# Kernel optimization log

Hardware: AMD Instinct MI355X
Metric: run time of the kernel (lower is better)

Reference implementation:

```python
import jax, jax.numpy as jnp
import numpy as np

BETA = 0.1
EPS_LOW = 0.2
EPS_HIGH = 0.2
TEMPERATURE = 1.0
H, V = 1024, 32000
B, T = 4, 1024


def _per_token_logps(hidden, weight, ids):
    # hidden: [B,T,H], weight: [V,H], ids: [B,T] -> gathered log-softmax logps [B,T]
    logits = jnp.einsum('bth,vh->btv', hidden, weight) / TEMPERATURE  # [B,T,V]
    lse = jax.nn.logsumexp(logits, axis=-1)                            # [B,T]
    sel = jnp.take_along_axis(logits, ids[..., None], axis=-1)[..., 0]
    return sel - lse


def setup_inputs() -> dict:
    key = jax.random.key(0)
    k1, k2, k3, k4, k5, k6 = jax.random.split(key, 6)
    x = jax.random.normal(k1, (B, T, H), dtype=jnp.float32)
    ref_input = jax.random.normal(k2, (B, T, H), dtype=jnp.float32)
    # lm-head weights (policy and frozen reference), scaled like nn.Linear init
    weight = jax.random.normal(k3, (V, H), dtype=jnp.float32) * (1.0 / np.sqrt(H))
    ref_weight = jax.random.normal(k4, (V, H), dtype=jnp.float32) * (1.0 / np.sqrt(H))
    selected_token_ids = jax.random.randint(k5, (B, T), 0, V, dtype=jnp.int32)
    attention_mask = jnp.ones((B, T), dtype=jnp.int32)
    advantages = jax.random.normal(k6, (B,), dtype=jnp.float32)
    return {
        'x': x,
        'weight': weight,
        'ref_input': ref_input,
        'ref_weight': ref_weight,
        'advantages': advantages,
        'selected_token_ids': selected_token_ids,
        'attention_mask': attention_mask,
    }


def reference(x, weight, ref_input, ref_weight, advantages, selected_token_ids, attention_mask):
    # policy per-token logps
    logps = _per_token_logps(x, weight, selected_token_ids)  # [B,T]
    # reference model logps (no grad path in original)
    ref_logps = jax.lax.stop_gradient(
        _per_token_logps(ref_input, ref_weight, selected_token_ids))
    # old logps default: detached current logps -> ratio = 1 in forward
    old_logps = jax.lax.stop_gradient(logps)

    log_ratio = logps - old_logps
    coef_1 = jnp.exp(log_ratio)
    coef_2 = jnp.clip(coef_1, 1.0 - EPS_LOW, 1.0 + EPS_HIGH)
    adv = advantages[:, None]  # [B,1]
    per_token_loss = -jnp.minimum(coef_1 * adv, coef_2 * adv)

    # KL penalty to reference model: exp(ref-cur) - (ref-cur) - 1
    d = ref_logps - logps
    kl = jnp.exp(d) - d - 1.0
    per_token_loss = per_token_loss + BETA * kl

    mask = attention_mask.astype(per_token_loss.dtype)
    # loss_type 'bnpo': batch-normalized policy optimization
    loss = jnp.sum(per_token_loss * mask) / jnp.maximum(jnp.sum(mask), 1.0)
    return loss
```

## Files before the change

### kernel.cpp

```cpp
#include <hip/hip_runtime.h>
#include <hip/hip_bf16.h>
#include <math.h>

constexpr int kH   = 1024;
constexpr int kV   = 32000;
constexpr int kTok = 4096;
constexpr int BM   = 256;
constexpr int BN   = 256;
constexpr int BK   = 64;
constexpr int NT   = kH / BK;
constexpr int NVT  = kV / BN;
constexpr int NMT  = kTok / BM;

typedef _Float16 f16x8 __attribute__((ext_vector_type(8)));
typedef float    f32x4 __attribute__((ext_vector_type(4)));

typedef __attribute__((address_space(1))) const void gvoid_t;
typedef __attribute__((address_space(3))) void lvoid_t;

__global__ __launch_bounds__(256) void convert_kernel(
    const float* __restrict__ src, _Float16* __restrict__ dst)
{
  int idx = blockIdx.x * 256 + threadIdx.x;
  int row = idx >> 7;
  int blk = idx & 127;
  int chunk = blk >> 3;
  int c = blk & 7;
  int p = c ^ (row & 7);
  const float* s = src + ((size_t)row << 10) + (blk << 3);
  float4 v0 = *(const float4*)s;
  float4 v1 = *(const float4*)(s + 4);
  f16x8 o = { (_Float16)v0.x, (_Float16)v0.y, (_Float16)v0.z, (_Float16)v0.w,
              (_Float16)v1.x, (_Float16)v1.y, (_Float16)v1.z, (_Float16)v1.w };
  *(f16x8*)&dst[((size_t)row << 10) + (chunk << 6) + (p << 3)] = o;
}

__global__ __launch_bounds__(512, 2) void lse_gemm_kernel(
    const _Float16* __restrict__ X0, const _Float16* __restrict__ W0,
    const _Float16* __restrict__ X1, const _Float16* __restrict__ W1,
    float2* __restrict__ P0, float2* __restrict__ P1)
{
  __shared__ _Float16 lds[2][2][BM * BK];

  const _Float16* Xp = blockIdx.z ? X1 : X0;
  const _Float16* Wp = blockIdx.z ? W1 : W0;
  float2* Pp = blockIdx.z ? P1 : P0;

  const int tid  = threadIdx.x;
  const int wave = tid >> 6;
  const int lane = tid & 63;
  const int quad = lane >> 4;
  const int lc   = lane & 15;
  const int wr   = wave >> 2;
  const int wc   = wave & 3;
  const int srow = lane >> 3;
  const int sblk = lane & 7;

  const int m_base = blockIdx.x * BM;
  const int v_base = blockIdx.y * BN;

  const _Float16* gA = Xp + (size_t)(m_base + wave * 8 + srow) * kH + sblk * 8;
  const _Float16* gB = Wp + (size_t)(v_base + wave * 8 + srow) * kH + sblk * 8;

  const int xb0 = ((quad       ^ (lc & 7)) << 3);
  const int xb1 = (((quad + 4) ^ (lc & 7)) << 3);
  const int rA0 = (wr * 128 + lc) * BK;
  const int rB0 = (wc * 64  + lc) * BK;

  f32x4 acc[8][4];
#pragma unroll
  for (int i = 0; i < 8; ++i)
#pragma unroll
    for (int j = 0; j < 4; ++j) acc[i][j] = (f32x4){0.f, 0.f, 0.f, 0.f};

  f16x8 bf[4][2];

#define STG_A(c, kt, h) do {                                                        \
    __builtin_amdgcn_global_load_lds(                                               \
        (gvoid_t*)(gA + (size_t)((h) * 128     ) * kH + (kt) * BK),                 \
        (lvoid_t*)&lds[c][0][(((h) * 128     ) + wave * 8) * BK], 16, 0, 0);        \
    __builtin_amdgcn_global_load_lds(                                               \
        (gvoid_t*)(gA + (size_t)((h) * 128 + 64) * kH + (kt) * BK),                 \
        (lvoid_t*)&lds[c][0][(((h) * 128 + 64) + wave * 8) * BK], 16, 0, 0);        \
  } while (0)
#define STG_B(c, kt, h) do {                                                        \
    __builtin_amdgcn_global_load_lds(                                               \
        (gvoid_t*)(gB + (size_t)((h) * 128     ) * kH + (kt) * BK),                 \
        (lvoid_t*)&lds[c][1][(((h) * 128     ) + wave * 8) * BK], 16, 0, 0);        \
    __builtin_amdgcn_global_load_lds(                                               \
        (gvoid_t*)(gB + (size_t)((h) * 128 + 64) * kH + (kt) * BK),                 \
        (lvoid_t*)&lds[c][1][(((h) * 128 + 64) + wave * 8) * BK], 16, 0, 0);        \
  } while (0)

#define VM6  asm volatile("s_waitcnt vmcnt(6)" ::: "memory")
#define VM0  asm volatile("s_waitcnt vmcnt(0)" ::: "memory")
#define NOP_ ((void)0)

#define PH(c, g, S, V) do {                                                         \
    if ((g) == 0) {                                                                 \
      _Pragma("unroll")                                                             \
      for (int j = 0; j < 4; ++j) {                                                 \
        bf[j][0] = *(const f16x8*)&lds[c][1][rB0 + j * 1024 + xb0];                 \
        bf[j][1] = *(const f16x8*)&lds[c][1][rB0 + j * 1024 + xb1];                 \
      }                                                                             \
    }                                                                               \
    f16x8 a00 = *(const f16x8*)&lds[c][0][rA0 + (g) * 2048 +        xb0];           \
    f16x8 a01 = *(const f16x8*)&lds[c][0][rA0 + (g) * 2048 +        xb1];           \
    f16x8 a10 = *(const f16x8*)&lds[c][0][rA0 + (g) * 2048 + 1024 + xb0];           \
    f16x8 a11 = *(const f16x8*)&lds[c][0][rA0 + (g) * 2048 + 1024 + xb1];           \
    S;                                                                              \
    V;                                                                              \
    __builtin_amdgcn_s_barrier();                                                   \
    __builtin_amdgcn_s_setprio(1);                                                  \
    _Pragma("unroll")                                                               \
    for (int j = 0; j < 4; ++j) {                                                   \
      acc[(g)*2  ][j] = __builtin_amdgcn_mfma_f32_16x16x32_f16(bf[j][0], a00, acc[(g)*2  ][j], 0, 0, 0); \
      acc[(g)*2  ][j] = __builtin_amdgcn_mfma_f32_16x16x32_f16(bf[j][1], a01, acc[(g)*2  ][j], 0, 0, 0); \
      acc[(g)*2+1][j] = __builtin_amdgcn_mfma_f32_16x16x32_f16(bf[j][0], a10, acc[(g)*2+1][j], 0, 0, 0); \
      acc[(g)*2+1][j] = __builtin_amdgcn_mfma_f32_16x16x32_f16(bf[j][1], a11, acc[(g)*2+1][j], 0, 0, 0); \
    }                                                                               \
    __builtin_amdgcn_s_setprio(0);                                                  \
    __builtin_amdgcn_s_barrier();                                                   \
  } while (0)

  STG_B(0, 0, 0); STG_B(0, 0, 1); STG_A(0, 0, 0); STG_A(0, 0, 1);
  STG_B(1, 1, 0); STG_B(1, 1, 1); STG_A(1, 1, 0);
  VM6;
  __builtin_amdgcn_s_barrier();

  for (int kt = 0; kt < NT - 2; kt += 2) {
    PH(0, 0, STG_A(1, kt + 1, 1), NOP_);
    PH(0, 1, STG_B(0, kt + 2, 0), NOP_);
    PH(0, 2, STG_B(0, kt + 2, 1), NOP_);
    PH(0, 3, STG_A(0, kt + 2, 0), VM6);
    PH(1, 0, STG_A(0, kt + 2, 1), NOP_);
    PH(1, 1, STG_B(1, kt + 3, 0), NOP_);
    PH(1, 2, STG_B(1, kt + 3, 1), NOP_);
    PH(1, 3, STG_A(1, kt + 3, 0), VM6);
  }
  PH(0, 0, STG_A(1, NT - 1, 1), NOP_);
  PH(0, 1, NOP_, NOP_);
  PH(0, 2, NOP_, NOP_);
  PH(0, 3, NOP_, VM0);
  PH(1, 0, NOP_, NOP_);
  PH(1, 1, NOP_, NOP_);
  PH(1, 2, NOP_, NOP_);
  PH(1, 3, NOP_, NOP_);

#undef PH
#undef STG_A
#undef STG_B

  float* redm = (float*)&lds[0][0][0];
  float* reds = redm + 4 * 256;

#pragma unroll
  for (int f = 0; f < 8; ++f) {
    float m = acc[f][0][0];
#pragma unroll
    for (int j = 0; j < 4; ++j)
#pragma unroll
      for (int r = 0; r < 4; ++r) m = fmaxf(m, acc[f][j][r]);
    float s = 0.f;
#pragma unroll
    for (int j = 0; j < 4; ++j)
#pragma unroll
      for (int r = 0; r < 4; ++r) s += __expf(acc[f][j][r] - m);
#pragma unroll
    for (int st = 16; st <= 32; st <<= 1) {
      float om = __shfl_xor(m, st, 64);
      float os = __shfl_xor(s, st, 64);
      float nm = fmaxf(m, om);
      s = s * __expf(m - nm) + os * __expf(om - nm);
      m = nm;
    }
    if (quad == 0) {
      int tok = wr * 128 + f * 16 + lc;
      redm[wc * 256 + tok] = m;
      reds[wc * 256 + tok] = s;
    }
  }
  __syncthreads();
  if (tid < 256) {
    float M = redm[tid], S = reds[tid];
#pragma unroll
    for (int w = 1; w < 4; ++w) {
      float m2 = redm[w * 256 + tid], s2 = reds[w * 256 + tid];
      float nm = fmaxf(M, m2);
      S = S * __expf(M - nm) + s2 * __expf(m2 - nm);
      M = nm;
    }
    Pp[(size_t)blockIdx.y * kTok + m_base + tid] = make_float2(M, S);
  }
}

__global__ __launch_bounds__(256) void sel_kernel(
    const float* __restrict__ X0, const float* __restrict__ W0,
    const float* __restrict__ X1, const float* __restrict__ W1,
    const int* __restrict__ ids, float* __restrict__ sel0, float* __restrict__ sel1)
{
  const int model = blockIdx.y;
  const float* X = model ? X1 : X0;
  const float* W = model ? W1 : W0;
  float* out = model ? sel1 : sel0;
  const int wave = threadIdx.x >> 6, lane = threadIdx.x & 63;
  const int t  = blockIdx.x * 4 + wave;
  const int id = ids[t];
  const float* xr = X + (size_t)t * kH;
  const float* wr = W + (size_t)id * kH;
  float s = 0.f;
#pragma unroll
  for (int r = 0; r < 4; ++r) {
    int idx = r * 256 + lane * 4;
    float4 a = *(const float4*)&xr[idx];
    float4 b = *(const float4*)&wr[idx];
    s += a.x * b.x + a.y * b.y + a.z * b.z + a.w * b.w;
  }
#pragma unroll
  for (int st = 32; st; st >>= 1) s += __shfl_xor(s, st, 64);
  if (lane == 0) out[t] = s;
}

__global__ __launch_bounds__(256) void finalize_kernel(
    const float2* __restrict__ P0, const float2* __restrict__ P1,
    const float* __restrict__ sel0, const float* __restrict__ sel1,
    const float* __restrict__ adv, const int* __restrict__ mask,
    float* __restrict__ accum)
{
  const int t = blockIdx.x * 256 + threadIdx.x;
  float M0 = -INFINITY, S0 = 0.f, M1 = -INFINITY, S1 = 0.f;
  for (int i = 0; i < NVT; ++i) {
    float2 p = P0[(size_t)i * kTok + t];
    if (p.x > M0) { S0 = S0 * __expf(M0 - p.x) + p.y; M0 = p.x; }
    else          { S0 += p.y * __expf(p.x - M0); }
  }
  for (int i = 0; i < NVT; ++i) {
    float2 p = P1[(size_t)i * kTok + t];
    if (p.x > M1) { S1 = S1 * __expf(M1 - p.x) + p.y; M1 = p.x; }
    else          { S1 += p.y * __expf(p.x - M1); }
  }
  float lse0  = M0 + logf(S0);
  float lse1  = M1 + logf(S1);
  float logp  = sel0[t] - lse0;
  float rlogp = sel1[t] - lse1;
  float d  = rlogp - logp;
  float kl = __expf(d) - d - 1.f;
  float a  = adv[t >> 10];
  float mv = (float)mask[t];
  float loss = (-a + 0.1f * kl) * mv;

#pragma unroll
  for (int st = 32; st; st >>= 1) {
    loss += __shfl_xor(loss, st, 64);
    mv   += __shfl_xor(mv, st, 64);
  }
  __shared__ float lsum[4], msum[4];
  const int wave = threadIdx.x >> 6, lane = threadIdx.x & 63;
  if (lane == 0) { lsum[wave] = loss; msum[wave] = mv; }
  __syncthreads();
  if (threadIdx.x == 0) {
    atomicAdd(&accum[0], lsum[0] + lsum[1] + lsum[2] + lsum[3]);
    atomicAdd(&accum[1], msum[0] + msum[1] + msum[2] + msum[3]);
  }
}

__global__ void scalar_kernel(const float* __restrict__ accum, float* __restrict__ out)
{
  out[0] = accum[0] / fmaxf(accum[1], 1.f);
}

extern "C" void kernel_launch(void* const* d_in, const int* in_sizes, int n_in,
                              void* d_out, int out_size, void* d_ws, size_t ws_size,
                              hipStream_t stream)
{
  const float* x    = (const float*)d_in[0];
  const float* w    = (const float*)d_in[1];
  const float* rx   = (const float*)d_in[2];
  const float* rw   = (const float*)d_in[3];
  const float* adv  = (const float*)d_in[4];
  const int*   ids  = (const int*)d_in[5];
  const int*   mask = (const int*)d_in[6];
  float* out = (float*)d_out;

  char* ws = (char*)d_ws;
  _Float16* Xh  = (_Float16*)ws;
  _Float16* Wh  = Xh + (size_t)kTok * kH;
  _Float16* RXh = Wh + (size_t)kV * kH;
  _Float16* RWh = RXh + (size_t)kTok * kH;
  float2*   P0  = (float2*)(RWh + (size_t)kV * kH);
  float2*   P1  = P0 + (size_t)NVT * kTok;
  float*    sel0 = (float*)(P1 + (size_t)NVT * kTok);
  float*    sel1 = sel0 + kTok;
  float*    accum = sel1 + kTok;

  hipMemsetAsync(accum, 0, 2 * sizeof(float), stream);

  convert_kernel<<<kTok * 128 / 256, 256, 0, stream>>>(x,  Xh);
  convert_kernel<<<kV   * 128 / 256, 256, 0, stream>>>(w,  Wh);
  convert_kernel<<<kTok * 128 / 256, 256, 0, stream>>>(rx, RXh);
  convert_kernel<<<kV   * 128 / 256, 256, 0, stream>>>(rw, RWh);

  sel_kernel<<<dim3(kTok / 4, 2), 256, 0, stream>>>(x, w, rx, rw, ids, sel0, sel1);

  lse_gemm_kernel<<<dim3(NMT, NVT, 2), 512, 0, stream>>>(Xh, Wh, RXh, RWh, P0, P1);

  finalize_kernel<<<kTok / 256, 256, 0, stream>>>(P0, P1, sel0, sel1, adv, mask, accum);
  scalar_kernel<<<1, 1, 0, stream>>>(accum, out);
}
```

Baseline: 863.0 us.

## Switch LSE GEMM to 32x32x16 MFMA with double-buffered A fragment reads

Replaces the 16x16x32 MFMA tiling with 32x32x16 MFMA instructions. Each wave now holds a 2x4 set of 16-float accumulators, and the vocab fragments are reused across four token sub-tiles. The A-fragment LDS reads are software-pipelined into alternating register sets so the next sub-tile's loads overlap the current MFMAs, and the epilogue reduction is rewritten for the new accumulator layout. The aim is fewer LDS reads per FLOP and better MFMA throughput, at the cost of more register pressure and extra barriers.

```diff
diff --git a/kernel.cpp b/kernel.cpp
--- a/kernel.cpp
+++ b/kernel.cpp
@@ -12,8 +12,8 @@
 constexpr int NVT  = kV / BN;
 constexpr int NMT  = kTok / BM;
 
-typedef _Float16 f16x8 __attribute__((ext_vector_type(8)));
-typedef float    f32x4 __attribute__((ext_vector_type(4)));
+typedef _Float16 f16x8  __attribute__((ext_vector_type(8)));
+typedef float    f32x16 __attribute__((ext_vector_type(16)));
 
 typedef __attribute__((address_space(1))) const void gvoid_t;
 typedef __attribute__((address_space(3))) void lvoid_t;
@@ -49,8 +49,9 @@
   const int tid  = threadIdx.x;
   const int wave = tid >> 6;
   const int lane = tid & 63;
-  const int quad = lane >> 4;
-  const int lc   = lane & 15;
+  const int l31  = lane & 31;
+  const int h    = lane >> 5;
+  const int ll7  = lane & 7;
   const int wr   = wave >> 2;
   const int wc   = wave & 3;
   const int srow = lane >> 3;
@@ -62,122 +63,125 @@
   const _Float16* gA = Xp + (size_t)(m_base + wave * 8 + srow) * kH + sblk * 8;
   const _Float16* gB = Wp + (size_t)(v_base + wave * 8 + srow) * kH + sblk * 8;
 
-  const int xb0 = ((quad       ^ (lc & 7)) << 3);
-  const int xb1 = (((quad + 4) ^ (lc & 7)) << 3);
-  const int rA0 = (wr * 128 + lc) * BK;
-  const int rB0 = (wc * 64  + lc) * BK;
-
-  f32x4 acc[8][4];
-#pragma unroll
-  for (int i = 0; i < 8; ++i)
-#pragma unroll
-    for (int j = 0; j < 4; ++j) acc[i][j] = (f32x4){0.f, 0.f, 0.f, 0.f};
-
-  f16x8 bf[4][2];
-
-#define STG_A(c, kt, h) do {                                                        \
+  const int baseA = (wr * 128 + l31) * BK;
+  const int baseV = (wc * 64  + l31) * BK;
+  int offK[4];
+#pragma unroll
+  for (int s = 0; s < 4; ++s) offK[s] = (((s * 2 + h) ^ ll7) << 3);
+
+  f32x16 acc[2][4];
+#pragma unroll
+  for (int j = 0; j < 2; ++j)
+#pragma unroll
+    for (int i = 0; i < 4; ++i)
+#pragma unroll
+      for (int r = 0; r < 16; ++r) acc[j][i][r] = 0.f;
+
+  f16x8 vf[2][4];
+  f16x8 tfa[4], tfb[4];
+
+#define STG_A(c, kt, hh) do {                                                       \
     __builtin_amdgcn_global_load_lds(                                               \
-        (gvoid_t*)(gA + (size_t)((h) * 128     ) * kH + (kt) * BK),                 \
-        (lvoid_t*)&lds[c][0][(((h) * 128     ) + wave * 8) * BK], 16, 0, 0);        \
+        (gvoid_t*)(gA + (size_t)((hh) * 128     ) * kH + (kt) * BK),                \
+        (lvoid_t*)&lds[c][0][(((hh) * 128     ) + wave * 8) * BK], 16, 0, 0);       \
     __builtin_amdgcn_global_load_lds(                                               \
-        (gvoid_t*)(gA + (size_t)((h) * 128 + 64) * kH + (kt) * BK),                 \
-        (lvoid_t*)&lds[c][0][(((h) * 128 + 64) + wave * 8) * BK], 16, 0, 0);        \
-  } while (0)
-#define STG_B(c, kt, h) do {                                                        \
+        (gvoid_t*)(gA + (size_t)((hh) * 128 + 64) * kH + (kt) * BK),                \
+        (lvoid_t*)&lds[c][0][(((hh) * 128 + 64) + wave * 8) * BK], 16, 0, 0);       \
+  } while (0)
+#define STG_B(c, kt, hh) do {                                                       \
     __builtin_amdgcn_global_load_lds(                                               \
-        (gvoid_t*)(gB + (size_t)((h) * 128     ) * kH + (kt) * BK),                 \
-        (lvoid_t*)&lds[c][1][(((h) * 128     ) + wave * 8) * BK], 16, 0, 0);        \
+        (gvoid_t*)(gB + (size_t)((hh) * 128     ) * kH + (kt) * BK),                \
+        (lvoid_t*)&lds[c][1][(((hh) * 128     ) + wave * 8) * BK], 16, 0, 0);       \
     __builtin_amdgcn_global_load_lds(                                               \
-        (gvoid_t*)(gB + (size_t)((h) * 128 + 64) * kH + (kt) * BK),                 \
-        (lvoid_t*)&lds[c][1][(((h) * 128 + 64) + wave * 8) * BK], 16, 0, 0);        \
-  } while (0)
-
+        (gvoid_t*)(gB + (size_t)((hh) * 128 + 64) * kH + (kt) * BK),                \
+        (lvoid_t*)&lds[c][1][(((hh) * 128 + 64) + wave * 8) * BK], 16, 0, 0);       \
+  } while (0)
+
+#define BAR do { asm volatile("" ::: "memory");                                     \
+                 __builtin_amdgcn_s_barrier();                                      \
+                 asm volatile("" ::: "memory"); } while (0)
 #define VM6  asm volatile("s_waitcnt vmcnt(6)" ::: "memory")
 #define VM0  asm volatile("s_waitcnt vmcnt(0)" ::: "memory")
-#define NOP_ ((void)0)
-
-#define PH(c, g, S, V) do {                                                         \
-    if ((g) == 0) {                                                                 \
+
+#define RDTF(dst, c, f) do {                                                        \
+    _Pragma("unroll")                                                               \
+    for (int s = 0; s < 4; ++s)                                                     \
+      dst[s] = *(const f16x8*)&lds[c][0][baseA + (f) * 2048 + offK[s]];             \
+  } while (0)
+#define RDVF(c) do {                                                                \
+    _Pragma("unroll")                                                               \
+    for (int j = 0; j < 2; ++j)                                                     \
       _Pragma("unroll")                                                             \
-      for (int j = 0; j < 4; ++j) {                                                 \
-        bf[j][0] = *(const f16x8*)&lds[c][1][rB0 + j * 1024 + xb0];                 \
-        bf[j][1] = *(const f16x8*)&lds[c][1][rB0 + j * 1024 + xb1];                 \
-      }                                                                             \
-    }                                                                               \
-    f16x8 a00 = *(const f16x8*)&lds[c][0][rA0 + (g) * 2048 +        xb0];           \
-    f16x8 a01 = *(const f16x8*)&lds[c][0][rA0 + (g) * 2048 +        xb1];           \
-    f16x8 a10 = *(const f16x8*)&lds[c][0][rA0 + (g) * 2048 + 1024 + xb0];           \
-    f16x8 a11 = *(const f16x8*)&lds[c][0][rA0 + (g) * 2048 + 1024 + xb1];           \
-    S;                                                                              \
-    V;                                                                              \
-    __builtin_amdgcn_s_barrier();                                                   \
+      for (int s = 0; s < 4; ++s)                                                   \
+        vf[j][s] = *(const f16x8*)&lds[c][1][baseV + j * 2048 + offK[s]];           \
+  } while (0)
+
+#define MM(g, TF) do {                                                              \
     __builtin_amdgcn_s_setprio(1);                                                  \
     _Pragma("unroll")                                                               \
-    for (int j = 0; j < 4; ++j) {                                                   \
-      acc[(g)*2  ][j] = __builtin_amdgcn_mfma_f32_16x16x32_f16(bf[j][0], a00, acc[(g)*2  ][j], 0, 0, 0); \
-      acc[(g)*2  ][j] = __builtin_amdgcn_mfma_f32_16x16x32_f16(bf[j][1], a01, acc[(g)*2  ][j], 0, 0, 0); \
-      acc[(g)*2+1][j] = __builtin_amdgcn_mfma_f32_16x16x32_f16(bf[j][0], a10, acc[(g)*2+1][j], 0, 0, 0); \
-      acc[(g)*2+1][j] = __builtin_amdgcn_mfma_f32_16x16x32_f16(bf[j][1], a11, acc[(g)*2+1][j], 0, 0, 0); \
+    for (int s = 0; s < 4; ++s) {                                                   \
+      acc[0][g] = __builtin_amdgcn_mfma_f32_32x32x16_f16(vf[0][s], TF[s], acc[0][g], 0, 0, 0); \
+      acc[1][g] = __builtin_amdgcn_mfma_f32_32x32x16_f16(vf[1][s], TF[s], acc[1][g], 0, 0, 0); \
     }                                                                               \
     __builtin_amdgcn_s_setprio(0);                                                  \
-    __builtin_amdgcn_s_barrier();                                                   \
   } while (0)
 
   STG_B(0, 0, 0); STG_B(0, 0, 1); STG_A(0, 0, 0); STG_A(0, 0, 1);
   STG_B(1, 1, 0); STG_B(1, 1, 1); STG_A(1, 1, 0);
   VM6;
-  __builtin_amdgcn_s_barrier();
+  BAR;
+  RDVF(0);
+  RDTF(tfa, 0, 0);
 
   for (int kt = 0; kt < NT - 2; kt += 2) {
-    PH(0, 0, STG_A(1, kt + 1, 1), NOP_);
-    PH(0, 1, STG_B(0, kt + 2, 0), NOP_);
-    PH(0, 2, STG_B(0, kt + 2, 1), NOP_);
-    PH(0, 3, STG_A(0, kt + 2, 0), VM6);
-    PH(1, 0, STG_A(0, kt + 2, 1), NOP_);
-    PH(1, 1, STG_B(1, kt + 3, 0), NOP_);
-    PH(1, 2, STG_B(1, kt + 3, 1), NOP_);
-    PH(1, 3, STG_A(1, kt + 3, 0), VM6);
-  }
-  PH(0, 0, STG_A(1, NT - 1, 1), NOP_);
-  PH(0, 1, NOP_, NOP_);
-  PH(0, 2, NOP_, NOP_);
-  PH(0, 3, NOP_, VM0);
-  PH(1, 0, NOP_, NOP_);
-  PH(1, 1, NOP_, NOP_);
-  PH(1, 2, NOP_, NOP_);
-  PH(1, 3, NOP_, NOP_);
-
-#undef PH
+    STG_A(1, kt + 1, 1); BAR; RDTF(tfb, 0, 1); MM(0, tfa); BAR;
+    STG_B(0, kt + 2, 0); BAR; RDTF(tfa, 0, 2); MM(1, tfb); BAR;
+    STG_B(0, kt + 2, 1); BAR; RDTF(tfb, 0, 3); MM(2, tfa); BAR;
+    STG_A(0, kt + 2, 0); VM6; BAR; RDTF(tfa, 1, 0); MM(3, tfb); RDVF(1); BAR;
+    STG_A(0, kt + 2, 1); BAR; RDTF(tfb, 1, 1); MM(0, tfa); BAR;
+    STG_B(1, kt + 3, 0); BAR; RDTF(tfa, 1, 2); MM(1, tfb); BAR;
+    STG_B(1, kt + 3, 1); BAR; RDTF(tfb, 1, 3); MM(2, tfa); BAR;
+    STG_A(1, kt + 3, 0); VM6; BAR; RDTF(tfa, 0, 0); MM(3, tfb); RDVF(0); BAR;
+  }
+
+  STG_A(1, NT - 1, 1); BAR; RDTF(tfb, 0, 1); MM(0, tfa); BAR;
+  BAR;                      RDTF(tfa, 0, 2); MM(1, tfb); BAR;
+  BAR;                      RDTF(tfb, 0, 3); MM(2, tfa); BAR;
+  VM0; BAR;                 RDTF(tfa, 1, 0); MM(3, tfb); RDVF(1); BAR;
+  BAR;                      RDTF(tfb, 1, 1); MM(0, tfa); BAR;
+  BAR;                      RDTF(tfa, 1, 2); MM(1, tfb); BAR;
+  BAR;                      RDTF(tfb, 1, 3); MM(2, tfa); BAR;
+  BAR;                                       MM(3, tfb);
+
 #undef STG_A
 #undef STG_B
+#undef RDTF
+#undef RDVF
+#undef MM
 
   float* redm = (float*)&lds[0][0][0];
   float* reds = redm + 4 * 256;
 
 #pragma unroll
-  for (int f = 0; f < 8; ++f) {
-    float m = acc[f][0][0];
-#pragma unroll
-    for (int j = 0; j < 4; ++j)
-#pragma unroll
-      for (int r = 0; r < 4; ++r) m = fmaxf(m, acc[f][j][r]);
+  for (int i = 0; i < 4; ++i) {
+    float m = acc[0][i][0];
+#pragma unroll
+    for (int r = 1; r < 16; ++r) m = fmaxf(m, acc[0][i][r]);
+#pragma unroll
+    for (int r = 0; r < 16; ++r) m = fmaxf(m, acc[1][i][r]);
     float s = 0.f;
 #pragma unroll
-    for (int j = 0; j < 4; ++j)
-#pragma unroll
-      for (int r = 0; r < 4; ++r) s += __expf(acc[f][j][r] - m);
-#pragma unroll
-    for (int st = 16; st <= 32; st <<= 1) {
-      float om = __shfl_xor(m, st, 64);
-      float os = __shfl_xor(s, st, 64);
-      float nm = fmaxf(m, om);
-      s = s * __expf(m - nm) + os * __expf(om - nm);
-      m = nm;
-    }
-    if (quad == 0) {
-      int tok = wr * 128 + f * 16 + lc;
-      redm[wc * 256 + tok] = m;
-      reds[wc * 256 + tok] = s;
+    for (int r = 0; r < 16; ++r) s += __expf(acc[0][i][r] - m);
+#pragma unroll
+    for (int r = 0; r < 16; ++r) s += __expf(acc[1][i][r] - m);
+    float om = __shfl_xor(m, 32, 64);
+    float os = __shfl_xor(s, 32, 64);
+    float nm = fmaxf(m, om);
+    s = s * __expf(m - nm) + os * __expf(om - nm);
+    m = nm;
+    if (lane < 32) {
+      redm[wc * 256 + wr * 128 + i * 32 + lane] = m;
+      reds[wc * 256 + wr * 128 + i * 32 + lane] = s;
     }
   }
   __syncthreads();
```

Result: slower. 916.4 us (+6.2%).
